# Kernel optimization log

Measured on AMD Instinct MI355X. Metric: run time of the kernel, lower is better.

Reference implementation:

```python
import jax, jax.numpy as jnp
import numpy as np

WINDOW = 20  # local attention window, per create_sparse_mask


def _make_mask(rng, n, sparsity_ratio=0.1):
    # local band: |i - j| <= window//2 (covers start/end clamping and the diagonal)
    idx = jnp.arange(n)
    mask = jnp.abs(idx[:, None] - idx[None, :]) <= (WINDOW // 2)
    # random edges: n_random (i, j) pairs set to 1 (duplicates harmless)
    n_random = int(sparsity_ratio * n * n)
    k1, k2 = jax.random.split(rng)
    ri = jax.random.randint(k1, (n_random,), 0, n)
    rj = jax.random.randint(k2, (n_random,), 0, n)
    mask = mask.at[ri, rj].set(True)
    return mask  # [n, n] bool


def setup_inputs() -> dict:
    rng = jax.random.key(0)
    kq, kk, kv, km = jax.random.split(rng, 4)
    B, H, S, D = 1, 8, 4096, 32
    return {
        "query": jax.random.normal(kq, (B, H, S, D), dtype=jnp.float32),
        "key": jax.random.normal(kk, (B, H, S, D), dtype=jnp.float32),
        "value": jax.random.normal(kv, (B, H, S, D), dtype=jnp.float32),
        "mask": _make_mask(km, S, sparsity_ratio=0.1),
    }


def reference(query, key, value, mask):
    # query/key/value: [B, H, S, D]; mask: [S, S] bool (True = attend)
    head_dim = query.shape[-1]
    scale = 1.0 / jnp.sqrt(jnp.float32(head_dim))
    scores = jnp.einsum("bhqd,bhkd->bhqk", query, key) * scale
    # torch: scores = scores * mask; masked_fill(mask == 0, -inf) -> equivalent to where
    scores = jnp.where(mask[None, None, :, :], scores, -jnp.inf)
    attn = jax.nn.softmax(scores, axis=-1)
    attn = jnp.nan_to_num(attn, nan=0.0)
    return jnp.einsum("bhqk,bhkd->bhqd", attn, value)
```

## Files before the change

kernel.cpp:

```cpp
#include <hip/hip_runtime.h>
#include <hip/hip_bf16.h>


#define S_  4096
#define D_  32
#define H_  8

typedef _Float16 half8 __attribute__((ext_vector_type(8)));
typedef __fp16 fp16x2 __attribute__((ext_vector_type(2)));
typedef short short8 __attribute__((ext_vector_type(8)));
typedef short short4v __attribute__((ext_vector_type(4)));
typedef float float4v __attribute__((ext_vector_type(4)));
typedef unsigned short ushort_t;
typedef unsigned int u32;

#if __has_builtin(__builtin_amdgcn_exp2f)
#define EXP2(x) __builtin_amdgcn_exp2f(x)
#else
#define EXP2(x) exp2f(x)
#endif

#if __has_builtin(__builtin_amdgcn_sbfe)
#define SEXT_BIT(v, b) ((u32)__builtin_amdgcn_sbfe((int)(v), (b), 1))
#else
#define SEXT_BIT(v, b) ((u32)(((int)((v) << (31 - (b)))) >> 31))
#endif

__device__ inline ushort_t f2h(float x) {
    union { _Float16 h; ushort_t u; } c; c.h = (_Float16)x; return c.u;
}

__global__ __launch_bounds__(256)
void prep_all(const float* __restrict__ Q, const float* __restrict__ K,
              const float* __restrict__ V, const int* __restrict__ mask,
              ushort_t* __restrict__ Qh, ushort_t* __restrict__ Kt,
              ushort_t* __restrict__ Vt, ushort_t* __restrict__ mlane)
{
    __shared__ u32 msh[16 * 257];
    const int bx = blockIdx.x;
    const int tid = threadIdx.x;
    union U8 { ushort_t u[8]; short8 v; };

    if (bx < 512) {
        const int e0 = (bx * 256 + tid) * 8;
        const float c = 0.17677669529663687f * 1.4426950408889634f;
        float4 a = *(const float4*)(Q + e0);
        float4 b = *(const float4*)(Q + e0 + 4);
        float f[8] = {a.x*c, a.y*c, a.z*c, a.w*c, b.x*c, b.y*c, b.z*c, b.w*c};
        U8 o;
#pragma unroll
        for (int i = 0; i < 8; ++i) o.u[i] = f2h(f[i]);
        *(short8*)(Qh + e0) = o.v;
    } else if (bx < 1024) {
        const int e0 = ((bx - 512) * 256 + tid) * 8;
        const int n = (e0 >> 3) & 15, quad = (e0 >> 7) & 3, t16 = (e0 >> 9) & 3;
        const int kt = (e0 >> 11) & 63, h = e0 >> 17;
        const int krow = kt * 64 + t16 * 16 + n;
        const float* src = K + ((size_t)h * S_ + krow) * D_ + quad * 8;
        float4 a = *(const float4*)src;
        float4 b = *(const float4*)(src + 4);
        float f[8] = {a.x, a.y, a.z, a.w, b.x, b.y, b.z, b.w};
        U8 o;
#pragma unroll
        for (int i = 0; i < 8; ++i) o.u[i] = f2h(f[i]);
        *(short8*)(Kt + e0) = o.v;
    } else if (bx < 1536) {
        const int e0 = ((bx - 1024) * 256 + tid) * 8;
        const int n = (e0 >> 3) & 15, quad = (e0 >> 7) & 3;
        const int dhalf = (e0 >> 9) & 1, khalf = (e0 >> 10) & 1;
        const int kt = (e0 >> 11) & 63, h = e0 >> 17;
        const int d = dhalf * 16 + n;
        U8 o;
#pragma unroll
        for (int j = 0; j < 8; ++j) {
            int krow = kt * 64 + khalf * 32 + (j >> 2) * 16 + quad * 4 + (j & 3);
            o.u[j] = f2h(V[((size_t)h * S_ + krow) * D_ + d]);
        }
        *(short8*)(Vt + e0) = o.v;
    } else {
        const int mb = bx - 1536;
        const int qt16 = mb >> 2, cc = mb & 3;
#pragma unroll
        for (int i = 0; i < 16; ++i) {
            int4 m4 = *(const int4*)(mask + (size_t)(qt16 * 16 + i) * S_ + cc * 1024 + tid * 4);
            u32 v = (m4.x != 0 ? 1u : 0u) | (m4.y != 0 ? 0x100u : 0u)
                  | (m4.z != 0 ? 0x10000u : 0u) | (m4.w != 0 ? 0x1000000u : 0u);
            msh[i * 257 + tid] = v;
        }
        __syncthreads();
        const int kt_local = tid >> 4, g = tid & 15;
        const int qd = g >> 2, n4 = g & 3;
        u32 o16[4] = {0, 0, 0, 0};
#pragma unroll
        for (int t16 = 0; t16 < 4; ++t16) {
            const int cbase = kt_local * 16 + t16 * 4 + qd;
#pragma unroll
            for (int b = 0; b < 4; ++b) {
                u32 v = msh[(n4 * 4 + b) * 257 + cbase];
                u32 nib = ((v * 0x01020408u) >> 24) & 0xFu;
                o16[b] |= nib << (t16 * 4);
            }
        }
        union { u32 w2[2]; short4v s; } pk;
        pk.w2[0] = o16[0] | (o16[1] << 16);
        pk.w2[1] = o16[2] | (o16[3] << 16);
        const int kt = cc * 16 + kt_local;
        *(short4v*)(mlane + ((size_t)(qt16 * 64 + kt) * 64 + g * 4)) = pk.s;
    }
}


__global__ __launch_bounds__(512, 4)
void attn_mfma(const ushort_t* __restrict__ Qh, const ushort_t* __restrict__ Kt,
               const ushort_t* __restrict__ Vt, const ushort_t* __restrict__ mlane,
               float* __restrict__ out)
{
    __shared__ __align__(16) float red[4 * (32 * 33 + 32)];
    const int RQ = 32 * 33 + 32;

    const int bid = blockIdx.x;
    const int swz = (bid & 7) * 128 + (bid >> 3);
    const int h  = swz >> 7;
    const int qb = swz & 127;
    const int q0 = qb * 32;

    const int tid = threadIdx.x;
    const int w = tid >> 6, l = tid & 63;
    const int n16 = l & 15, quad = l >> 4;

    const ushort_t* mlw = mlane + ((size_t)(qb * 2) << 12);

    half8 qh[2];
#pragma unroll
    for (int qs = 0; qs < 2; ++qs)
        qh[qs] = *(const half8*)(Qh + ((size_t)h * S_ + q0 + qs * 16 + n16) * D_ + quad * 8);

    half8 ones;
#pragma unroll
    for (int i = 0; i < 8; ++i) ones[i] = (_Float16)1.0f;

    float4v o0[2], o1[2], lacc[2];
#pragma unroll
    for (int qs = 0; qs < 2; ++qs) {
        o0[qs] = (float4v){0.f, 0.f, 0.f, 0.f};
        o1[qs] = (float4v){0.f, 0.f, 0.f, 0.f};
        lacc[qs] = (float4v){0.f, 0.f, 0.f, 0.f};
    }

    const int fo = quad * 128 + n16 * 8;
    const ushort_t* Ktp = Kt + (size_t)h * 64 * 2048;
    const ushort_t* Vtp = Vt + (size_t)h * 64 * 2048;

    const int kt0 = w * 8;

    half8 kb[2][4], vv[2][4];
    u32 mm[2][2];

#define LOADT(p, kt) { \
    const ushort_t* tb = Ktp + (kt) * 2048; \
    const ushort_t* vb = Vtp + (kt) * 2048; \
    mm[p][0] = mlw[(kt) * 64 + l]; \
    mm[p][1] = mlw[4096 + (kt) * 64 + l]; \
    kb[p][0] = *(const half8*)(tb + fo); \
    kb[p][1] = *(const half8*)(tb + 512 + fo); \
    kb[p][2] = *(const half8*)(tb + 1024 + fo); \
    kb[p][3] = *(const half8*)(tb + 1536 + fo); \
    vv[p][0] = *(const half8*)(vb + fo); \
    vv[p][1] = *(const half8*)(vb + 512 + fo); \
    vv[p][2] = *(const half8*)(vb + 1024 + fo); \
    vv[p][3] = *(const half8*)(vb + 1536 + fo); \
}

#define COMPUTE(p) { \
    _Pragma("unroll") \
    for (int kh = 0; kh < 2; ++kh) { \
        _Pragma("unroll") \
        for (int qs = 0; qs < 2; ++qs) { \
            float4v c0 = {0.f, 0.f, 0.f, 0.f}; \
            float4v c1 = {0.f, 0.f, 0.f, 0.f}; \
            c0 = __builtin_amdgcn_mfma_f32_16x16x32_f16(kb[p][2*kh],   qh[qs], c0, 0, 0, 0); \
            c1 = __builtin_amdgcn_mfma_f32_16x16x32_f16(kb[p][2*kh+1], qh[qs], c1, 0, 0, 0); \
            float f0[4], f1[4]; \
            _Pragma("unroll") \
            for (int r = 0; r < 4; ++r) { \
                float e0 = EXP2(c0[r]); \
                float e1 = EXP2(c1[r]); \
                u32 k0 = SEXT_BIT(mm[p][qs], kh * 8 + r); \
                u32 k1 = SEXT_BIT(mm[p][qs], kh * 8 + 4 + r); \
                f0[r] = __uint_as_float(__float_as_uint(e0) & k0); \
                f1[r] = __uint_as_float(__float_as_uint(e1) & k1); \
            } \
            union { fp16x2 hh[4]; half8 h8; } pk; \
            pk.hh[0] = __builtin_amdgcn_cvt_pkrtz(f0[0], f0[1]); \
            pk.hh[1] = __builtin_amdgcn_cvt_pkrtz(f0[2], f0[3]); \
            pk.hh[2] = __builtin_amdgcn_cvt_pkrtz(f1[0], f1[1]); \
            pk.hh[3] = __builtin_amdgcn_cvt_pkrtz(f1[2], f1[3]); \
            const half8 pa = pk.h8; \
            o0[qs]   = __builtin_amdgcn_mfma_f32_16x16x32_f16(pa, vv[p][2*kh],   o0[qs],   0, 0, 0); \
            o1[qs]   = __builtin_amdgcn_mfma_f32_16x16x32_f16(pa, vv[p][2*kh+1], o1[qs],   0, 0, 0); \
            lacc[qs] = __builtin_amdgcn_mfma_f32_16x16x32_f16(pa, ones, lacc[qs], 0, 0, 0); \
        } \
    } \
}

    LOADT(0, kt0 + 0);
    for (int i = 0; i < 6; i += 2) {
        LOADT(1, kt0 + i + 1);
        COMPUTE(0);
        __builtin_amdgcn_sched_barrier(0);
        LOADT(0, kt0 + i + 2);
        COMPUTE(1);
        __builtin_amdgcn_sched_barrier(0);
    }
    LOADT(1, kt0 + 7);
    COMPUTE(0);
    __builtin_amdgcn_sched_barrier(0);
    COMPUTE(1);

#undef LOADT
#undef COMPUTE

#define DUMP(slot) { \
    float* ro = red + (slot) * RQ; \
    _Pragma("unroll") for (int qs = 0; qs < 2; ++qs) \
    _Pragma("unroll") for (int r = 0; r < 4; ++r) { \
        const int q = qs * 16 + quad * 4 + r; \
        ro[q * 33 + n16]      = o0[qs][r]; \
        ro[q * 33 + 16 + n16] = o1[qs][r]; \
        if (n16 == 0) ro[32 * 33 + q] = lacc[qs][r]; \
    } }
#define ADDIN(slot) { \
    const float* ro = red + (slot) * RQ; \
    _Pragma("unroll") for (int qs = 0; qs < 2; ++qs) \
    _Pragma("unroll") for (int r = 0; r < 4; ++r) { \
        const int q = qs * 16 + quad * 4 + r; \
        o0[qs][r]   += ro[q * 33 + n16]; \
        o1[qs][r]   += ro[q * 33 + 16 + n16]; \
        lacc[qs][r] += ro[32 * 33 + q]; \
    } }

    if (w >= 4) DUMP(w - 4);
    __syncthreads();
    if (w < 4) ADDIN(w);
    __syncthreads();
    if (w == 2 || w == 3) DUMP(w - 2);
    __syncthreads();
    if (w < 2) ADDIN(w);
    __syncthreads();
    if (w == 1) DUMP(0);
    __syncthreads();
    if (w == 0) {
        const float* ro = red + 0 * RQ;
#pragma unroll
        for (int qs = 0; qs < 2; ++qs)
#pragma unroll
            for (int r = 0; r < 4; ++r) {
                const int q = qs * 16 + quad * 4 + r;
                const float s0 = o0[qs][r] + ro[q * 33 + n16];
                const float s1 = o1[qs][r] + ro[q * 33 + 16 + n16];
                const float sl = lacc[qs][r] + ro[32 * 33 + q];
                const float inv = 1.0f / sl;
                float* orow = out + ((size_t)h * S_ + q0 + q) * D_;
                orow[n16]      = s0 * inv;
                orow[16 + n16] = s1 * inv;
            }
    }
#undef DUMP
#undef ADDIN
}


#define QT 64
#define KT 64
#define NSUB 4
#define KPT 16

__global__ __launch_bounds__(256, 2)
void sparse_attn_fp32(const float* __restrict__ Q, const float* __restrict__ K,
                      const float* __restrict__ V, const int* __restrict__ mask,
                      float* __restrict__ out)
{
    __shared__ float Ks[KT][D_];
    __shared__ float Vs[KT][D_];
    __shared__ float red_o[NSUB][QT][D_ + 1];
    __shared__ float red_l[NSUB][QT];

    const int h = blockIdx.y;
    const int q0 = blockIdx.x * QT;
    const int tid = threadIdx.x;
    const int ql = tid & 63;
    const int sub = tid >> 6;
    const int q = q0 + ql;
    const float scale = 0.17677669529663687f;

    float4 qreg[8];
    const float4* qrow = (const float4*)(Q + ((size_t)h * S_ + q) * D_);
#pragma unroll
    for (int i = 0; i < 8; ++i) qreg[i] = qrow[i];

    float o[D_];
#pragma unroll
    for (int d = 0; d < D_; ++d) o[d] = 0.f;
    float lsum0 = 0.f;

    const float* Kh = K + (size_t)h * S_ * D_;
    const float* Vh = V + (size_t)h * S_ * D_;

    for (int jt = 0; jt < S_; jt += KT) {
        __syncthreads();
        {
            const float4* gK = (const float4*)(Kh + (size_t)jt * D_);
            const float4* gV = (const float4*)(Vh + (size_t)jt * D_);
            float4* sK = (float4*)&Ks[0][0];
            float4* sV = (float4*)&Vs[0][0];
            sK[tid] = gK[tid]; sK[tid + 256] = gK[tid + 256];
            sV[tid] = gV[tid]; sV[tid + 256] = gV[tid + 256];
        }
        __syncthreads();

        int4 m4[4];
        {
            const int4* mr = (const int4*)(mask + (size_t)q * S_ + jt + sub * KPT);
#pragma unroll
            for (int i = 0; i < 4; ++i) m4[i] = mr[i];
        }
        const int* mb = (const int*)m4;

#pragma unroll
        for (int kk = 0; kk < KPT; ++kk) {
            const int jl = sub * KPT + kk;
            const float4* krow = (const float4*)&Ks[jl][0];
            float s = 0.f;
#pragma unroll
            for (int i = 0; i < 8; ++i) {
                float4 kv = krow[i];
                s += qreg[i].x * kv.x + qreg[i].y * kv.y + qreg[i].z * kv.z + qreg[i].w * kv.w;
            }
            const float p = mb[kk] ? __expf(s * scale) : 0.f;
            lsum0 += p;
            const float4* vrow = (const float4*)&Vs[jl][0];
#pragma unroll
            for (int i = 0; i < 8; ++i) {
                float4 vv = vrow[i];
                o[i * 4 + 0] += p * vv.x;
                o[i * 4 + 1] += p * vv.y;
                o[i * 4 + 2] += p * vv.z;
                o[i * 4 + 3] += p * vv.w;
            }
        }
    }

#pragma unroll
    for (int d = 0; d < D_; ++d) red_o[sub][ql][d] = o[d];
    red_l[sub][ql] = lsum0;
    __syncthreads();

    const int eq = tid & 63;
    const int dg = tid >> 6;
    float acc[8];
#pragma unroll
    for (int i = 0; i < 8; ++i) acc[i] = 0.f;
    float lsum = 0.f;
#pragma unroll
    for (int s2 = 0; s2 < NSUB; ++s2) {
        lsum += red_l[s2][eq];
#pragma unroll
        for (int i = 0; i < 8; ++i) acc[i] += red_o[s2][eq][dg * 8 + i];
    }
    const float inv = 1.0f / lsum;
    float* orow = out + ((size_t)h * S_ + q0 + eq) * D_ + dg * 8;
#pragma unroll
    for (int i = 0; i < 8; ++i) orow[i] = acc[i] * inv;
}


extern "C" void kernel_launch(void* const* d_in, const int* in_sizes, int n_in,
                              void* d_out, int out_size, void* d_ws, size_t ws_size,
                              hipStream_t stream) {
    const float* Q = (const float*)d_in[0];
    const float* K = (const float*)d_in[1];
    const float* V = (const float*)d_in[2];
    const int* mask = (const int*)d_in[3];
    float* out = (float*)d_out;

    const size_t MB = 1024 * 1024;
    if (ws_size < 8 * MB) {
        dim3 grid(S_ / QT, H_);
        sparse_attn_fp32<<<grid, 256, 0, stream>>>(Q, K, V, mask, out);
        return;
    }

    char* ws = (char*)d_ws;
    ushort_t* Qh = (ushort_t*)(ws + 0 * MB);
    ushort_t* Kt = (ushort_t*)(ws + 2 * MB);
    ushort_t* Vt = (ushort_t*)(ws + 4 * MB);
    ushort_t* mlane = (ushort_t*)(ws + 6 * MB);

    prep_all<<<2560, 256, 0, stream>>>(Q, K, V, mask, Qh, Kt, Vt, mlane);
    attn_mfma<<<1024, 512, 0, stream>>>(Qh, Kt, Vt, mlane, out);
}
```

Measured before the change: 136.3 us.

## Replace tree reduction with single-barrier all-wave reduction and prioritize MFMA compute

```diff
diff --git a/kernel.cpp b/kernel.cpp
--- a/kernel.cpp
+++ b/kernel.cpp
@@ -115,7 +115,7 @@
                const ushort_t* __restrict__ Vt, const ushort_t* __restrict__ mlane,
                float* __restrict__ out)
 {
-    __shared__ __align__(16) float red[4 * (32 * 33 + 32)];
+    __shared__ __align__(16) float red[8 * (32 * 33 + 32)];
     const int RQ = 32 * 33 + 32;
 
     const int bid = blockIdx.x;
@@ -172,6 +172,7 @@
 }
 
 #define COMPUTE(p) { \
+    __builtin_amdgcn_s_setprio(1); \
     _Pragma("unroll") \
     for (int kh = 0; kh < 2; ++kh) { \
         _Pragma("unroll") \
@@ -201,6 +202,7 @@
             lacc[qs] = __builtin_amdgcn_mfma_f32_16x16x32_f16(pa, ones, lacc[qs], 0, 0, 0); \
         } \
     } \
+    __builtin_amdgcn_s_setprio(0); \
 }
 
     LOADT(0, kt0 + 0);
@@ -220,53 +222,34 @@
 #undef LOADT
 #undef COMPUTE
 
-#define DUMP(slot) { \
-    float* ro = red + (slot) * RQ; \
-    _Pragma("unroll") for (int qs = 0; qs < 2; ++qs) \
-    _Pragma("unroll") for (int r = 0; r < 4; ++r) { \
-        const int q = qs * 16 + quad * 4 + r; \
-        ro[q * 33 + n16]      = o0[qs][r]; \
-        ro[q * 33 + 16 + n16] = o1[qs][r]; \
-        if (n16 == 0) ro[32 * 33 + q] = lacc[qs][r]; \
-    } }
-#define ADDIN(slot) { \
-    const float* ro = red + (slot) * RQ; \
-    _Pragma("unroll") for (int qs = 0; qs < 2; ++qs) \
-    _Pragma("unroll") for (int r = 0; r < 4; ++r) { \
-        const int q = qs * 16 + quad * 4 + r; \
-        o0[qs][r]   += ro[q * 33 + n16]; \
-        o1[qs][r]   += ro[q * 33 + 16 + n16]; \
-        lacc[qs][r] += ro[32 * 33 + q]; \
-    } }
-
-    if (w >= 4) DUMP(w - 4);
-    __syncthreads();
-    if (w < 4) ADDIN(w);
-    __syncthreads();
-    if (w == 2 || w == 3) DUMP(w - 2);
-    __syncthreads();
-    if (w < 2) ADDIN(w);
-    __syncthreads();
-    if (w == 1) DUMP(0);
-    __syncthreads();
-    if (w == 0) {
-        const float* ro = red + 0 * RQ;
+    {
+        float* ro = red + w * RQ;
 #pragma unroll
         for (int qs = 0; qs < 2; ++qs)
 #pragma unroll
             for (int r = 0; r < 4; ++r) {
                 const int q = qs * 16 + quad * 4 + r;
-                const float s0 = o0[qs][r] + ro[q * 33 + n16];
-                const float s1 = o1[qs][r] + ro[q * 33 + 16 + n16];
-                const float sl = lacc[qs][r] + ro[32 * 33 + q];
-                const float inv = 1.0f / sl;
-                float* orow = out + ((size_t)h * S_ + q0 + q) * D_;
-                orow[n16]      = s0 * inv;
-                orow[16 + n16] = s1 * inv;
+                ro[q * 33 + n16]      = o0[qs][r];
+                ro[q * 33 + 16 + n16] = o1[qs][r];
+                if (n16 == 0) ro[32 * 33 + q] = lacc[qs][r];
             }
     }
-#undef DUMP
-#undef ADDIN
+    __syncthreads();
+    {
+        const int q = tid >> 4, d = tid & 15;
+        float s0 = 0.f, s1 = 0.f, sl = 0.f;
+#pragma unroll
+        for (int s = 0; s < 8; ++s) {
+            const float* ro = red + s * RQ;
+            s0 += ro[q * 33 + d];
+            s1 += ro[q * 33 + 16 + d];
+            sl += ro[32 * 33 + q];
+        }
+        const float inv = 1.0f / sl;
+        float* orow = out + ((size_t)h * S_ + q0 + q) * D_;
+        orow[d]      = s0 * inv;
+        orow[16 + d] = s1 * inv;
+    }
 }
 
 
```

New measurement: 148.3 us. 8.8% more time.
